# Optimization experiments

Measured on AMD Instinct MI355X. Metric: run time of the kernel, lower is better.

## Reference

```python
import jax, jax.numpy as jnp
import numpy as np

A_NUM = 9
C_NUM = 20

def setup_inputs() -> dict:
    key = jax.random.key(0)
    ks = jax.random.split(key, 12)
    B, Cin, H, W = 32, 256, 56, 56
    hidden = 256
    N, M = 64, 2048
    out_ch = 5 * A_NUM + C_NUM
    features = jax.random.normal(ks[0], (B, Cin, H, W), jnp.float32)
    w1 = jax.random.normal(ks[1], (hidden, Cin), jnp.float32) * (1.0 / np.sqrt(Cin))
    b1 = jax.random.normal(ks[2], (hidden,), jnp.float32) * 0.01
    w2 = jax.random.normal(ks[3], (out_ch, hidden), jnp.float32) * (1.0 / np.sqrt(hidden))
    b2 = jax.random.normal(ks[4], (out_ch,), jnp.float32) * 0.01
    # anchor shapes (w, h), positive sizes in grid units
    anc = 1.0 + 5.0 * jax.random.uniform(ks[5], (A_NUM, 2), jnp.float32)
    # grid of cell centers
    xs = jnp.arange(W, dtype=jnp.float32) + 0.5
    ys = jnp.arange(H, dtype=jnp.float32) + 0.5
    gx, gy = jnp.meshgrid(xs, ys, indexing='xy')  # (H, W)
    grid = jnp.broadcast_to(jnp.stack([gx, gy], axis=-1)[None], (B, H, W, 2))
    # GT boxes (x1, y1, x2, y2, cls) with x1<x2, y1<y2
    x1 = jax.random.uniform(ks[6], (B, N), jnp.float32) * (W - 9.0)
    y1 = jax.random.uniform(ks[7], (B, N), jnp.float32) * (H - 9.0)
    bw = 1.0 + 7.0 * jax.random.uniform(ks[8], (B, N), jnp.float32)
    bh = 1.0 + 7.0 * jax.random.uniform(ks[9], (B, N), jnp.float32)
    cls = jax.random.randint(ks[10], (B, N), 0, C_NUM).astype(jnp.float32)
    bboxes = jnp.stack([x1, y1, x1 + bw, y1 + bh, cls], axis=-1)
    total_anchors = B * A_NUM * H * W
    pos_anchor_idx = jax.random.randint(ks[11], (M,), 0, total_anchors, jnp.int64 if jax.config.jax_enable_x64 else jnp.int32)
    neg_anchor_idx = jax.random.randint(jax.random.fold_in(key, 99), (M,), 0, total_anchors, jnp.int64 if jax.config.jax_enable_x64 else jnp.int32)
    GT_offsets = jax.random.normal(jax.random.fold_in(key, 100), (M, 4), jnp.float32) * 0.1
    return {"features": features, "w1": w1, "b1": b1, "w2": w2, "b2": b2,
            "anc": anc, "grid": grid, "bboxes": bboxes, "GT_offsets": GT_offsets,
            "pos_anchor_idx": pos_anchor_idx, "neg_anchor_idx": neg_anchor_idx}

def _generate_anchor(anc, grid):
    # grid: (B,H,W,2), anc: (A,2) -> anchors (B,A,H,W,4) as (x1,y1,x2,y2)
    g = grid[:, None]                      # (B,1,H,W,2)
    a = anc[None, :, None, None]           # (1,A,1,1,2)
    return jnp.concatenate([g - a / 2, g + a / 2], axis=-1)

def _generate_proposal_yolo(anchors, offsets):
    ctr = (anchors[..., :2] + anchors[..., 2:]) / 2
    wh = anchors[..., 2:] - anchors[..., :2]
    new_wh = wh * jnp.exp(offsets[..., 2:])
    new_ctr = ctr + offsets[..., :2]
    return jnp.concatenate([new_ctr - new_wh / 2, new_ctr + new_wh / 2], axis=-1)

def _iou(proposals, bboxes):
    # proposals (B,A,H,W,4) -> (B,AHW,4); bboxes (B,N,5) -> iou (B,AHW,N)
    B = proposals.shape[0]
    p = proposals.reshape(B, -1, 4)[:, :, None, :]   # (B,AHW,1,4)
    g = bboxes[:, None, :, :]                        # (B,1,N,5)
    ix1 = jnp.maximum(p[..., 0], g[..., 0])
    iy1 = jnp.maximum(p[..., 1], g[..., 1])
    ix2 = jnp.minimum(p[..., 2], g[..., 2])
    iy2 = jnp.minimum(p[..., 3], g[..., 3])
    inter = jnp.clip(ix2 - ix1, 0) * jnp.clip(iy2 - iy1, 0)
    gt_area = (bboxes[:, :, 2] - bboxes[:, :, 0]) * (bboxes[:, :, 3] - bboxes[:, :, 1])
    p_area = (p[..., 2] - p[..., 0]) * (p[..., 3] - p[..., 1])
    return inter / (gt_area[:, None, :] + p_area - inter)

def reference(features, w1, b1, w2, b2, anc, grid, bboxes, GT_offsets,
              pos_anchor_idx, neg_anchor_idx):
    B, _, H, W = features.shape
    A = anc.shape[0]
    M = pos_anchor_idx.shape[0]
    # PredictionNetwork (dropout in eval = identity), 1x1 convs as einsum
    x = jnp.einsum('bchw,oc->bohw', features, w1) + b1[None, :, None, None]
    x = jax.nn.leaky_relu(x, 0.01)
    x = jnp.einsum('bchw,oc->bohw', x, w2) + b2[None, :, None, None]
    anc_data = x[:, :5 * A].reshape(B, A, 5, H, W)
    class_all = x[:, 5 * A:]                               # (B,C,H,W)
    conf_all = jax.nn.sigmoid(anc_data[:, :, 0])           # (B,A,H,W)
    offsets_all = jnp.transpose(anc_data[:, :, 1:5], (0, 1, 3, 4, 2))  # (B,A,H,W,4)
    # training extraction
    conf_flat = conf_all.reshape(-1)
    conf_scores = jnp.concatenate([conf_flat[pos_anchor_idx], conf_flat[neg_anchor_idx]])[:, None]  # (2M,1)
    offsets_pos = offsets_all.reshape(-1, 4)[pos_anchor_idx]            # (M,4)
    # class scores for positive anchors: index arithmetic over (B,A,H,W)
    bi = pos_anchor_idx // (A * H * W)
    hw = pos_anchor_idx % (H * W)
    hi, wi = hw // W, hw % W
    class_pos = class_all[bi, :, hi, wi]                                # (M,C)
    # anchors -> proposals -> IoU
    anchors = _generate_anchor(anc, grid)
    proposals = _generate_proposal_yolo(anchors, offsets_all)
    iou_mat = _iou(proposals, bboxes)                                   # (B,AHW,N)
    # YOLO SSE losses
    gt_conf = jnp.concatenate([jnp.ones((M, 1), conf_scores.dtype), jnp.zeros((M, 1), conf_scores.dtype)])
    conf_loss = jnp.sum((conf_scores - gt_conf) ** 2) / (2 * M)
    reg_loss = jnp.sum((offsets_pos - GT_offsets) ** 2) / M
    total_loss = conf_loss + reg_loss
    return total_loss, iou_mat, class_pos
```

## Files before the change

kernel.cpp:

```cpp
#include <hip/hip_runtime.h>
#include <math.h>

#define B_    32
#define CIN   256
#define HID   256
#define OC    65
#define A_    9
#define H_    56
#define W_    56
#define HW    3136
#define AHW   28224
#define NBOX  64
#define M_    2048
#define CNUM  20
#define NTILE 49
#define NTILES_TOT (B_ * NTILE)
#define NSLOT 25

#define IOU_N ((size_t)B_ * AHW * NBOX)

#define WS_W1S   0
#define WS_W2S   131072
#define WS_LOSS  172032
#define WS_PCNT  172288
#define WS_NCNT  178560
#define WS_PBUF  184832
#define WS_NBUF  586240

#define FOFF(frag) (((frag) << 3) + ((((frag) >> 3)) << 3))

typedef _Float16 half8 __attribute__((ext_vector_type(8)));
typedef float f32x16 __attribute__((ext_vector_type(16)));
typedef float f32x4  __attribute__((ext_vector_type(4)));

__device__ __forceinline__ unsigned int pkh(float a, float b) {
    _Float16 ha = (_Float16)a, hb = (_Float16)b;
    unsigned short ua = __builtin_bit_cast(unsigned short, ha);
    unsigned short ub = __builtin_bit_cast(unsigned short, hb);
    return (unsigned int)ua | ((unsigned int)ub << 16);
}

__device__ __forceinline__ void phase_barrier() {
    __builtin_amdgcn_sched_barrier(0);
    asm volatile("s_waitcnt lgkmcnt(0)" ::: "memory");
    __builtin_amdgcn_s_barrier();
    __builtin_amdgcn_sched_barrier(0);
}

__global__ __launch_bounds__(256) void zero_kernel(int* __restrict__ cnts,
                                                   float* __restrict__ loss_ws) {
    const int i = blockIdx.x * 256 + threadIdx.x;
    if (i < 2 * NTILES_TOT) cnts[i] = 0;
    if (i < 2) loss_ws[i] = 0.f;
}

__global__ __launch_bounds__(256) void prep_kernel(
    const float* __restrict__ w1, const float* __restrict__ w2,
    _Float16* __restrict__ w1s, _Float16* __restrict__ w2s,
    const int* __restrict__ pos_idx, const int* __restrict__ neg_idx,
    int* __restrict__ pcnt, int* __restrict__ ncnt,
    int* __restrict__ pbuf, int* __restrict__ nbuf)
{
    const int f = blockIdx.x * 256 + threadIdx.x;
    {
        const int e    = f & 7;
        const int lane = (f >> 3) & 63;
        const int kc   = (f >> 9) & 15;
        const int ob   = f >> 13;
        const int row  = ob * 32 + (lane & 31);
        const int k    = kc * 16 + (lane >> 5) * 8 + e;
        w1s[f] = (_Float16)w1[row * CIN + k];
    }
    if (f < 20480) {
        const int e    = f & 7;
        const int lane = (f >> 3) & 63;
        const int ks2  = (f >> 9) & 7;
        const int rt   = f >> 12;
        const int row  = rt * 16 + (lane & 15);
        const int k    = ks2 * 32 + (lane >> 4) * 8 + e;
        w2s[f] = (row < OC) ? (_Float16)w2[row * HID + k] : (_Float16)0.f;
    }
    if (f < 2 * M_) {
        const int m   = f & (M_ - 1);
        const int idx = (f < M_) ? pos_idx[m] : neg_idx[m];
        const int bi  = idx / AHW;
        const int rr  = idx - bi * AHW;
        const int a   = rr / HW;
        const int hw  = rr - a * HW;
        const int tile = bi * NTILE + (hw >> 6);
        const int enc  = m | (a << 11) | ((hw & 63) << 15);
        if (f < M_) {
            const int s = atomicAdd(&pcnt[tile], 1);
            if (s < 64) pbuf[tile * 64 + s] = enc;
        } else {
            const int s = atomicAdd(&ncnt[tile], 1);
            if (s < 64) nbuf[tile * 64 + s] = enc;
        }
    }
}

__device__ __forceinline__ void stage_issue(const float* __restrict__ fbase,
                                            int kk, int pstage,
                                            float4* __restrict__ s0,
                                            float4* __restrict__ s1)
{
#pragma unroll
    for (int c = 0; c < 8; ++c) {
        s0[c] = *(const float4*)(fbase + (size_t)(c * 32 + kk) * HW + pstage);
        s1[c] = *(const float4*)(fbase + (size_t)(c * 32 + kk + 1) * HW + pstage);
    }
}

__device__ __forceinline__ void stage_store(_Float16* __restrict__ featAll,
                                            int pstage, int ksS, int gS, int j0h,
                                            const float4* __restrict__ s0,
                                            const float4* __restrict__ s1)
{
#pragma unroll
    for (int c = 0; c < 8; ++c) {
        const float a0[4] = {s0[c].x, s0[c].y, s0[c].z, s0[c].w};
        const float a1[4] = {s1[c].x, s1[c].y, s1[c].z, s1[c].w};
#pragma unroll
        for (int e = 0; e < 4; ++e) {
            const int p     = pstage + e;
            const int lane2 = gS * 32 + (p & 31);
            const int pt    = p >> 5;
            const int frag  = c * 256 + (ksS * 2 + pt) * 64 + lane2;
            *(unsigned int*)&featAll[FOFF(frag) + j0h] = pkh(a0[e], a1[e]);
        }
    }
}

__global__ __launch_bounds__(256) void conv_iou_kernel(
    const float* __restrict__ features, const _Float16* __restrict__ w1s,
    const float* __restrict__ b1, const _Float16* __restrict__ w2s,
    const float* __restrict__ b2, const float* __restrict__ anc,
    const float* __restrict__ bboxes,
    const int* __restrict__ pcnt, const int* __restrict__ ncnt,
    const int* __restrict__ pbuf, const int* __restrict__ nbuf,
    const float* __restrict__ gt_off,
    float* __restrict__ iou_out, float* __restrict__ cls_out,
    float* __restrict__ loss_ws)
{
    __shared__ _Float16 lds_h[18432];
    __shared__ float bias_s[HID];
    __shared__ float boxs[5 * 64];
    __shared__ float red[8];

    _Float16* featAll = lds_h;
    _Float16* hidf    = lds_h;
    float*    L       = (float*)lds_h;
    float*    x2t     = L;

    const int t    = threadIdx.x;
    const int lane = t & 63;
    const int w    = t >> 6;
    const int bid  = blockIdx.x;
    const int b    = bid / NSLOT;
    const int slot = bid - b * NSLOT;
    const int j0t  = slot * 2;
    const int ntiles = (slot < NSLOT - 1) ? 2 : 1;
    const float* fb0 = features + (size_t)b * CIN * HW;

    float* WPw = L + 4416 + w * 720;

    bias_s[t] = b1[t];
    if (t < 64) {
        const float* gb = bboxes + ((size_t)b * NBOX + t) * 5;
        const float x1 = gb[0], y1 = gb[1], x2v = gb[2], y2v = gb[3];
        boxs[t] = x1; boxs[64 + t] = y1; boxs[128 + t] = x2v; boxs[192 + t] = y2v;
        boxs[256 + t] = (x2v - x1) * (y2v - y1);
    }

    const int pstage = (t & 15) * 4;
    const int kk     = (t >> 4) * 2;
    const int ksS    = kk >> 4;
    const int gS     = (kk >> 3) & 1;
    const int j0h    = kk & 7;
    const int ghalf  = lane >> 5;
    const int col    = lane & 31;
    const int m16    = lane & 15;
    const int kgr    = lane >> 4;
    const int pr     = lane >> 4;
    const int j0     = (lane & 15) * 4;

    float Bx1[4], By1[4], Bx2[4], By2[4], Ba[4];

    float4 s0[8], s1[8];
    stage_issue(fb0 + j0t * 64, kk, pstage, s0, s1);

    float csum = 0.f, rsum = 0.f;

    for (int it = 0; it < ntiles; ++it) {
        const int p0 = (j0t + it) * 64;

        stage_store(featAll, pstage, ksS, gS, j0h, s0, s1);
        phase_barrier();

        if (it == 0) {
#pragma unroll
            for (int e = 0; e < 4; ++e) {
                Bx1[e] = boxs[j0 + e];       By1[e] = boxs[64 + j0 + e];
                Bx2[e] = boxs[128 + j0 + e]; By2[e] = boxs[192 + j0 + e];
                Ba[e]  = boxs[256 + j0 + e];
            }
        }

        f32x16 facc[2][2];
#pragma unroll
        for (int ot = 0; ot < 2; ++ot)
#pragma unroll
            for (int pt = 0; pt < 2; ++pt)
#pragma unroll
                for (int e = 0; e < 16; ++e) facc[ot][pt][e] = 0.f;

        half8 afb[2][2][2];
#pragma unroll
        for (int ks = 0; ks < 2; ++ks)
#pragma unroll
            for (int ot = 0; ot < 2; ++ot)
                afb[0][ks][ot] = *(const half8*)(w1s + ((size_t)((w * 2 + ot) * 16 + ks) * 64 + lane) * 8);

#pragma unroll
        for (int c = 0; c < 8; ++c) {
            if (c < 7) {
#pragma unroll
                for (int ks = 0; ks < 2; ++ks)
#pragma unroll
                    for (int ot = 0; ot < 2; ++ot)
                        afb[(c + 1) & 1][ks][ot] =
                            *(const half8*)(w1s + ((size_t)((w * 2 + ot) * 16 + (c + 1) * 2 + ks) * 64 + lane) * 8);
            }
#pragma unroll
            for (int ks = 0; ks < 2; ++ks) {
#pragma unroll
                for (int pt = 0; pt < 2; ++pt) {
                    const half8 bf = *(const half8*)&featAll[FOFF(c * 256 + (ks * 2 + pt) * 64 + lane)];
                    facc[0][pt] = __builtin_amdgcn_mfma_f32_32x32x16_f16(afb[c & 1][ks][0], bf, facc[0][pt], 0, 0, 0);
                    facc[1][pt] = __builtin_amdgcn_mfma_f32_32x32x16_f16(afb[c & 1][ks][1], bf, facc[1][pt], 0, 0, 0);
                }
            }
        }
        phase_barrier();

#pragma unroll
        for (int ot = 0; ot < 2; ++ot) {
            const int ks2 = w * 2 + ot;
#pragma unroll
            for (int pt = 0; pt < 2; ++pt) {
                const int pt2 = pt * 2 + (col >> 4);
                const int n15 = col & 15;
#pragma unroll
                for (int q = 0; q < 4; ++q) {
                    float hv[4];
#pragma unroll
                    for (int i = 0; i < 4; ++i) {
                        const int row = i + 8 * q + 4 * ghalf;
                        float v = facc[ot][pt][q * 4 + i] + bias_s[w * 64 + ot * 32 + row];
                        hv[i] = v < 0.f ? 0.01f * v : v;
                    }
                    const int frag = (ks2 * 4 + pt2) * 64 + (q * 16 + n15);
                    *(unsigned int*)&hidf[FOFF(frag) + 4 * ghalf]     = pkh(hv[0], hv[1]);
                    *(unsigned int*)&hidf[FOFF(frag) + 4 * ghalf + 2] = pkh(hv[2], hv[3]);
                }
            }
        }
        phase_barrier();

        f32x4 c2[5];
#pragma unroll
        for (int rt = 0; rt < 5; ++rt)
#pragma unroll
            for (int e = 0; e < 4; ++e) c2[rt][e] = 0.f;

        half8 afc[2][5];
#pragma unroll
        for (int rt = 0; rt < 5; ++rt)
            afc[0][rt] = *(const half8*)(w2s + ((size_t)(rt * 8) * 64 + lane) * 8);

#pragma unroll
        for (int ks2 = 0; ks2 < 8; ++ks2) {
            if (ks2 < 7) {
#pragma unroll
                for (int rt = 0; rt < 5; ++rt)
                    afc[(ks2 + 1) & 1][rt] =
                        *(const half8*)(w2s + ((size_t)(rt * 8 + ks2 + 1) * 64 + lane) * 8);
            }
            const half8 bf = *(const half8*)&hidf[FOFF((ks2 * 4 + w) * 64 + lane)];
#pragma unroll
            for (int rt = 0; rt < 5; ++rt)
                c2[rt] = __builtin_amdgcn_mfma_f32_16x16x32_f16(afc[ks2 & 1][rt], bf, c2[rt], 0, 0, 0);
        }

        if (it + 1 < ntiles)
            stage_issue(fb0 + (p0 + 64), kk, pstage, s0, s1);

        phase_barrier();

        const int pxl = w * 16 + m16;
#pragma unroll
        for (int rt = 0; rt < 5; ++rt) {
#pragma unroll
            for (int r = 0; r < 4; ++r) {
                const int o2 = rt * 16 + kgr * 4 + r;
                if (o2 < OC) x2t[pxl * 69 + o2] = c2[rt][r] + b2[o2];
            }
        }
        asm volatile("" ::: "memory");

        for (int i = lane; i < A_ * 16; i += 64) {
            const int a  = i >> 4;
            const int pw = i & 15;
            const float* xr = x2t + (w * 16 + pw) * 69 + 5 * a;
            const float tx = xr[1], ty = xr[2], tw = xr[3], th = xr[4];
            const int hwg = p0 + w * 16 + pw;
            const int h   = hwg / W_;
            const int wv  = hwg - h * W_;
            const float gx = (float)wv + 0.5f;
            const float gy = (float)h + 0.5f;
            const float nw = anc[2 * a]     * __expf(tw);
            const float nh = anc[2 * a + 1] * __expf(th);
            const float cx = gx + tx, cy = gy + ty;
            WPw[i]       = cx - 0.5f * nw;
            WPw[144 + i] = cy - 0.5f * nh;
            WPw[288 + i] = cx + 0.5f * nw;
            WPw[432 + i] = cy + 0.5f * nh;
            WPw[576 + i] = nw * nh;
        }
        asm volatile("" ::: "memory");

        float* ibase = iou_out + ((size_t)b * AHW + p0) * 64;
#pragma unroll 1
        for (int a = 0; a < A_; ++a) {
            float Px1[4], Py1[4], Px2[4], Py2[4], Pa[4];
#pragma unroll
            for (int q = 0; q < 4; ++q) {
                const int idx = a * 16 + q * 4 + pr;
                Px1[q] = WPw[idx];       Py1[q] = WPw[144 + idx];
                Px2[q] = WPw[288 + idx]; Py2[q] = WPw[432 + idx];
                Pa[q]  = WPw[576 + idx];
            }
#pragma unroll
            for (int q = 0; q < 4; ++q) {
                f32x4 o4;
#pragma unroll
                for (int e = 0; e < 4; ++e) {
                    const float iw = fminf(Px2[q], Bx2[e]) - fmaxf(Px1[q], Bx1[e]);
                    const float ih = fminf(Py2[q], By2[e]) - fmaxf(Py1[q], By1[e]);
                    const float inter = fmaxf(iw, 0.f) * fmaxf(ih, 0.f);
                    o4[e] = inter * __builtin_amdgcn_rcpf(Ba[e] + Pa[q] - inter);
                }
                *(f32x4*)(ibase + ((size_t)(a * HW) + w * 16 + q * 4 + pr) * 64 + j0) = o4;
            }
        }

        phase_barrier();

        {
            const int bidt = b * NTILE + j0t + it;
            int np = pcnt[bidt]; np = np > 64 ? 64 : np;
            for (int i = t; i < np; i += 256) {
                const int e  = pbuf[bidt * 64 + i];
                const int m  = e & 2047;
                const int a  = (e >> 11) & 15;
                const int px = (e >> 15) & 63;
                const float* xr = x2t + px * 69;
                const float s = 1.f / (1.f + __expf(-xr[5 * a]));
                csum += (s - 1.f) * (s - 1.f);
#pragma unroll
                for (int k = 0; k < 4; ++k) {
                    const float d = xr[5 * a + 1 + k] - gt_off[m * 4 + k];
                    rsum += d * d;
                }
                float* co = cls_out + (size_t)m * CNUM;
#pragma unroll
                for (int c = 0; c < CNUM; ++c) co[c] = xr[45 + c];
            }
            int nn = ncnt[bidt]; nn = nn > 64 ? 64 : nn;
            for (int i = t; i < nn; i += 256) {
                const int e  = nbuf[bidt * 64 + i];
                const int a  = (e >> 11) & 15;
                const int px = (e >> 15) & 63;
                const float s = 1.f / (1.f + __expf(-x2t[px * 69 + 5 * a]));
                csum += s * s;
            }
        }
        phase_barrier();
    }

#pragma unroll
    for (int off = 32; off > 0; off >>= 1) {
        csum += __shfl_down(csum, off, 64);
        rsum += __shfl_down(rsum, off, 64);
    }
    if (lane == 0) { red[w] = csum; red[4 + w] = rsum; }
    __syncthreads();
    if (t == 0) {
        const float c  = red[0] + red[1] + red[2] + red[3];
        const float rg = red[4] + red[5] + red[6] + red[7];
        if (c != 0.f || rg != 0.f) {
            atomicAdd(&loss_ws[0], c);
            atomicAdd(&loss_ws[1], rg);
        }
    }
}

__global__ void finalize_kernel(const float* __restrict__ loss_ws, float* __restrict__ out0)
{
    out0[0] = loss_ws[0] / (2.f * (float)M_) + loss_ws[1] / (float)M_;
}

extern "C" void kernel_launch(void* const* d_in, const int* in_sizes, int n_in,
                              void* d_out, int out_size, void* d_ws, size_t ws_size,
                              hipStream_t stream) {
    (void)in_sizes; (void)n_in; (void)out_size; (void)ws_size;
    const float* features = (const float*)d_in[0];
    const float* w1       = (const float*)d_in[1];
    const float* b1       = (const float*)d_in[2];
    const float* w2       = (const float*)d_in[3];
    const float* b2       = (const float*)d_in[4];
    const float* anc      = (const float*)d_in[5];
    const float* bboxes   = (const float*)d_in[7];
    const float* gt_off   = (const float*)d_in[8];
    const int*   pos_idx  = (const int*)d_in[9];
    const int*   neg_idx  = (const int*)d_in[10];
    float* out = (float*)d_out;

    char* wsb = (char*)d_ws;
    _Float16* w1s  = (_Float16*)(wsb + WS_W1S);
    _Float16* w2s  = (_Float16*)(wsb + WS_W2S);
    float* loss_ws = (float*)(wsb + WS_LOSS);
    int*   pcnt    = (int*)(wsb + WS_PCNT);
    int*   ncnt    = (int*)(wsb + WS_NCNT);
    int*   pbuf    = (int*)(wsb + WS_PBUF);
    int*   nbuf    = (int*)(wsb + WS_NBUF);

    zero_kernel<<<13, 256, 0, stream>>>(pcnt, loss_ws);
    prep_kernel<<<256, 256, 0, stream>>>(w1, w2, w1s, w2s, pos_idx, neg_idx,
                                         pcnt, ncnt, pbuf, nbuf);
    conv_iou_kernel<<<B_ * NSLOT, 256, 0, stream>>>(features, w1s, b1, w2s, b2,
                                                    anc, bboxes, pcnt, ncnt, pbuf, nbuf,
                                                    gt_off, out + 1,
                                                    out + 1 + IOU_N, loss_ws);
    finalize_kernel<<<1, 1, 0, stream>>>(loss_ws, out);
}
```

Before: 432.3 us.

## Restructure fused conv kernel to one tile per block with per-wave pixel split

Each block now handles a single 64-pixel tile (1568 blocks) rather than two tiles with software prefetch of the next tile's features. Layer 1 switches from 32x32 MFMAs split over output channels to 16x16x32 MFMAs where each wave owns 16 pixels and all 256 hidden channels. The hidden activations are passed to layer 2 through cross-lane shuffles in registers, which removes the LDS round trip and several block barriers. The feature staging layout gains an XOR swizzle to cut LDS bank conflicts. In exchange, each wave now reads all of W1 from global/L2 with no double buffering, and per-thread register pressure rises from 64 accumulators.

```diff
diff --git a/kernel.cpp b/kernel.cpp
--- a/kernel.cpp
+++ b/kernel.cpp
@@ -15,7 +15,6 @@
 #define CNUM  20
 #define NTILE 49
 #define NTILES_TOT (B_ * NTILE)
-#define NSLOT 25
 
 #define IOU_N ((size_t)B_ * AHW * NBOX)
 
@@ -27,10 +26,7 @@
 #define WS_PBUF  184832
 #define WS_NBUF  586240
 
-#define FOFF(frag) (((frag) << 3) + ((((frag) >> 3)) << 3))
-
 typedef _Float16 half8 __attribute__((ext_vector_type(8)));
-typedef float f32x16 __attribute__((ext_vector_type(16)));
 typedef float f32x4  __attribute__((ext_vector_type(4)));
 
 __device__ __forceinline__ unsigned int pkh(float a, float b) {
@@ -40,12 +36,7 @@
     return (unsigned int)ua | ((unsigned int)ub << 16);
 }
 
-__device__ __forceinline__ void phase_barrier() {
-    __builtin_amdgcn_sched_barrier(0);
-    asm volatile("s_waitcnt lgkmcnt(0)" ::: "memory");
-    __builtin_amdgcn_s_barrier();
-    __builtin_amdgcn_sched_barrier(0);
-}
+__device__ __forceinline__ int swz(int h) { return h ^ (((h >> 12) & 3) << 4); }
 
 __global__ __launch_bounds__(256) void zero_kernel(int* __restrict__ cnts,
                                                    float* __restrict__ loss_ws) {
@@ -65,10 +56,10 @@
     {
         const int e    = f & 7;
         const int lane = (f >> 3) & 63;
-        const int kc   = (f >> 9) & 15;
-        const int ob   = f >> 13;
-        const int row  = ob * 32 + (lane & 31);
-        const int k    = kc * 16 + (lane >> 5) * 8 + e;
+        const int ks   = (f >> 9) & 7;
+        const int rt   = (f >> 12) & 15;
+        const int row  = rt * 16 + (lane & 15);
+        const int k    = ks * 32 + (lane >> 4) * 8 + e;
         w1s[f] = (_Float16)w1[row * CIN + k];
     }
     if (f < 20480) {
@@ -99,38 +90,6 @@
     }
 }
 
-__device__ __forceinline__ void stage_issue(const float* __restrict__ fbase,
-                                            int kk, int pstage,
-                                            float4* __restrict__ s0,
-                                            float4* __restrict__ s1)
-{
-#pragma unroll
-    for (int c = 0; c < 8; ++c) {
-        s0[c] = *(const float4*)(fbase + (size_t)(c * 32 + kk) * HW + pstage);
-        s1[c] = *(const float4*)(fbase + (size_t)(c * 32 + kk + 1) * HW + pstage);
-    }
-}
-
-__device__ __forceinline__ void stage_store(_Float16* __restrict__ featAll,
-                                            int pstage, int ksS, int gS, int j0h,
-                                            const float4* __restrict__ s0,
-                                            const float4* __restrict__ s1)
-{
-#pragma unroll
-    for (int c = 0; c < 8; ++c) {
-        const float a0[4] = {s0[c].x, s0[c].y, s0[c].z, s0[c].w};
-        const float a1[4] = {s1[c].x, s1[c].y, s1[c].z, s1[c].w};
-#pragma unroll
-        for (int e = 0; e < 4; ++e) {
-            const int p     = pstage + e;
-            const int lane2 = gS * 32 + (p & 31);
-            const int pt    = p >> 5;
-            const int frag  = c * 256 + (ksS * 2 + pt) * 64 + lane2;
-            *(unsigned int*)&featAll[FOFF(frag) + j0h] = pkh(a0[e], a1[e]);
-        }
-    }
-}
-
 __global__ __launch_bounds__(256) void conv_iou_kernel(
     const float* __restrict__ features, const _Float16* __restrict__ w1s,
     const float* __restrict__ b1, const _Float16* __restrict__ w2s,
@@ -142,29 +101,22 @@
     float* __restrict__ iou_out, float* __restrict__ cls_out,
     float* __restrict__ loss_ws)
 {
-    __shared__ _Float16 lds_h[18432];
-    __shared__ float bias_s[HID];
+    __shared__ _Float16 lds_h[16384];
     __shared__ float boxs[5 * 64];
     __shared__ float red[8];
 
-    _Float16* featAll = lds_h;
-    _Float16* hidf    = lds_h;
-    float*    L       = (float*)lds_h;
-    float*    x2t     = L;
+    float* LF = (float*)lds_h;
 
     const int t    = threadIdx.x;
     const int lane = t & 63;
     const int w    = t >> 6;
+    const int g    = lane >> 4;
+    const int m16  = lane & 15;
     const int bid  = blockIdx.x;
-    const int b    = bid / NSLOT;
-    const int slot = bid - b * NSLOT;
-    const int j0t  = slot * 2;
-    const int ntiles = (slot < NSLOT - 1) ? 2 : 1;
-    const float* fb0 = features + (size_t)b * CIN * HW;
-
-    float* WPw = L + 4416 + w * 720;
-
-    bias_s[t] = b1[t];
+    const int b    = bid / NTILE;
+    const int p0   = (bid - b * NTILE) * 64;
+    const float* fbase = features + (size_t)b * CIN * HW + p0;
+
     if (t < 64) {
         const float* gb = bboxes + ((size_t)b * NBOX + t) * 5;
         const float x1 = gb[0], y1 = gb[1], x2v = gb[2], y2v = gb[3];
@@ -174,220 +126,192 @@
 
     const int pstage = (t & 15) * 4;
     const int kk     = (t >> 4) * 2;
-    const int ksS    = kk >> 4;
-    const int gS     = (kk >> 3) & 1;
-    const int j0h    = kk & 7;
-    const int ghalf  = lane >> 5;
-    const int col    = lane & 31;
-    const int m16    = lane & 15;
-    const int kgr    = lane >> 4;
-    const int pr     = lane >> 4;
-    const int j0     = (lane & 15) * 4;
-
+#pragma unroll
+    for (int hf = 0; hf < 2; ++hf) {
+        float4 r0[4], r1[4];
+#pragma unroll
+        for (int c4 = 0; c4 < 4; ++c4) {
+            const int c = hf * 4 + c4;
+            r0[c4] = *(const float4*)(fbase + (size_t)(c * 32 + kk) * HW + pstage);
+            r1[c4] = *(const float4*)(fbase + (size_t)(c * 32 + kk + 1) * HW + pstage);
+        }
+#pragma unroll
+        for (int c4 = 0; c4 < 4; ++c4) {
+            const int c = hf * 4 + c4;
+            const float a0[4] = {r0[c4].x, r0[c4].y, r0[c4].z, r0[c4].w};
+            const float a1[4] = {r1[c4].x, r1[c4].y, r1[c4].z, r1[c4].w};
+#pragma unroll
+            for (int e = 0; e < 4; ++e) {
+                const int p = pstage + e;
+                const int W = ((p >> 4) * 8 + c) * 512
+                            + (((kk >> 3) & 3) * 16 + (p & 15)) * 8 + (kk & 7);
+                *(unsigned int*)&lds_h[swz(W)] = pkh(a0[e], a1[e]);
+            }
+        }
+    }
+    __syncthreads();
+
+    f32x4 facc[16];
+#pragma unroll
+    for (int rt = 0; rt < 16; ++rt)
+#pragma unroll
+        for (int e = 0; e < 4; ++e) facc[rt][e] = 0.f;
+
+#pragma unroll
+    for (int ks = 0; ks < 8; ++ks) {
+        const half8 bf = *(const half8*)&lds_h[swz(((w * 8 + ks) * 64 + lane) * 8)];
+#pragma unroll
+        for (int rt = 0; rt < 16; ++rt) {
+            const half8 af = *(const half8*)(w1s + ((size_t)(rt * 8 + ks) * 64 + lane) * 8);
+            facc[rt] = __builtin_amdgcn_mfma_f32_16x16x32_f16(af, bf, facc[rt], 0, 0, 0);
+        }
+    }
+
+    unsigned hvpk[8][4];
+#pragma unroll
+    for (int rt2 = 0; rt2 < 8; ++rt2) {
+        const float4 bA = *(const float4*)(b1 + (2 * rt2) * 16 + g * 4);
+        const float4 bB = *(const float4*)(b1 + (2 * rt2 + 1) * 16 + g * 4);
+        const float bav[4] = {bA.x, bA.y, bA.z, bA.w};
+        const float bbv[4] = {bB.x, bB.y, bB.z, bB.w};
+#pragma unroll
+        for (int r = 0; r < 4; ++r) {
+            float va = facc[2 * rt2][r] + bav[r];
+            float vb = facc[2 * rt2 + 1][r] + bbv[r];
+            va = va < 0.f ? 0.01f * va : va;
+            vb = vb < 0.f ? 0.01f * vb : vb;
+            hvpk[rt2][r] = pkh(va, vb);
+        }
+    }
+
+    f32x4 c2[5];
+#pragma unroll
+    for (int rt = 0; rt < 5; ++rt)
+#pragma unroll
+        for (int e = 0; e < 4; ++e) c2[rt][e] = 0.f;
+
+    const int src0 = (g & 1) * 32 + m16;
+    const int sh   = (g >> 1) * 16;
+#pragma unroll
+    for (int ks2 = 0; ks2 < 8; ++ks2) {
+        unsigned u[8];
+#pragma unroll
+        for (int j = 0; j < 8; ++j)
+            u[j] = (unsigned)__shfl((int)hvpk[ks2][j & 3], (j < 4) ? src0 : src0 + 16);
+        union { unsigned q[4]; half8 h; } bu;
+#pragma unroll
+        for (int wd = 0; wd < 4; ++wd)
+            bu.q[wd] = ((u[2 * wd] >> sh) & 0xffffu) | (((u[2 * wd + 1] >> sh) & 0xffffu) << 16);
+#pragma unroll
+        for (int rt = 0; rt < 5; ++rt) {
+            const half8 af = *(const half8*)(w2s + ((size_t)(rt * 8 + ks2) * 64 + lane) * 8);
+            c2[rt] = __builtin_amdgcn_mfma_f32_16x16x32_f16(af, bu.h, c2[rt], 0, 0, 0);
+        }
+    }
+    asm volatile("" ::: "memory");
+
+    float* xw = LF + w * 2048;
+#pragma unroll
+    for (int rt = 0; rt < 5; ++rt) {
+#pragma unroll
+        for (int r = 0; r < 4; ++r) {
+            const int o2 = rt * 16 + g * 4 + r;
+            if (o2 < OC) xw[m16 * 69 + o2] = c2[rt][r] + b2[o2];
+        }
+    }
+    asm volatile("" ::: "memory");
+
+    float* WPw = LF + w * 2048 + 1104;
+    for (int i = lane; i < A_ * 16; i += 64) {
+        const int a  = i >> 4;
+        const int pw = i & 15;
+        const float* xr = xw + pw * 69 + 5 * a;
+        const float tx = xr[1], ty = xr[2], tw = xr[3], th = xr[4];
+        const int hwg = p0 + w * 16 + pw;
+        const int h   = hwg / W_;
+        const int wv  = hwg - h * W_;
+        const float gx = (float)wv + 0.5f;
+        const float gy = (float)h + 0.5f;
+        const float nw = anc[2 * a]     * __expf(tw);
+        const float nh = anc[2 * a + 1] * __expf(th);
+        const float cx = gx + tx, cy = gy + ty;
+        WPw[i]       = cx - 0.5f * nw;
+        WPw[144 + i] = cy - 0.5f * nh;
+        WPw[288 + i] = cx + 0.5f * nw;
+        WPw[432 + i] = cy + 0.5f * nh;
+        WPw[576 + i] = nw * nh;
+    }
+    asm volatile("" ::: "memory");
+
+    const int pr = g;
+    const int j0 = m16 * 4;
     float Bx1[4], By1[4], Bx2[4], By2[4], Ba[4];
-
-    float4 s0[8], s1[8];
-    stage_issue(fb0 + j0t * 64, kk, pstage, s0, s1);
+#pragma unroll
+    for (int e = 0; e < 4; ++e) {
+        Bx1[e] = boxs[j0 + e];       By1[e] = boxs[64 + j0 + e];
+        Bx2[e] = boxs[128 + j0 + e]; By2[e] = boxs[192 + j0 + e];
+        Ba[e]  = boxs[256 + j0 + e];
+    }
+    float* ibase = iou_out + ((size_t)b * AHW + p0) * 64;
+#pragma unroll 1
+    for (int a = 0; a < A_; ++a) {
+        float Px1[4], Py1[4], Px2[4], Py2[4], Pa[4];
+#pragma unroll
+        for (int q = 0; q < 4; ++q) {
+            const int idx = a * 16 + q * 4 + pr;
+            Px1[q] = WPw[idx];       Py1[q] = WPw[144 + idx];
+            Px2[q] = WPw[288 + idx]; Py2[q] = WPw[432 + idx];
+            Pa[q]  = WPw[576 + idx];
+        }
+#pragma unroll
+        for (int q = 0; q < 4; ++q) {
+            f32x4 o4;
+#pragma unroll
+            for (int e = 0; e < 4; ++e) {
+                const float iw = fminf(Px2[q], Bx2[e]) - fmaxf(Px1[q], Bx1[e]);
+                const float ih = fminf(Py2[q], By2[e]) - fmaxf(Py1[q], By1[e]);
+                const float inter = fmaxf(iw, 0.f) * fmaxf(ih, 0.f);
+                o4[e] = inter * __builtin_amdgcn_rcpf(Ba[e] + Pa[q] - inter);
+            }
+            *(f32x4*)(ibase + ((size_t)(a * HW) + w * 16 + q * 4 + pr) * 64 + j0) = o4;
+        }
+    }
+
+    __builtin_amdgcn_sched_barrier(0);
+    asm volatile("s_waitcnt lgkmcnt(0)" ::: "memory");
+    __builtin_amdgcn_s_barrier();
+    __builtin_amdgcn_sched_barrier(0);
 
     float csum = 0.f, rsum = 0.f;
-
-    for (int it = 0; it < ntiles; ++it) {
-        const int p0 = (j0t + it) * 64;
-
-        stage_store(featAll, pstage, ksS, gS, j0h, s0, s1);
-        phase_barrier();
-
-        if (it == 0) {
-#pragma unroll
-            for (int e = 0; e < 4; ++e) {
-                Bx1[e] = boxs[j0 + e];       By1[e] = boxs[64 + j0 + e];
-                Bx2[e] = boxs[128 + j0 + e]; By2[e] = boxs[192 + j0 + e];
-                Ba[e]  = boxs[256 + j0 + e];
+    {
+        int np = pcnt[bid]; np = np > 64 ? 64 : np;
+        for (int i = t; i < np; i += 256) {
+            const int e  = pbuf[bid * 64 + i];
+            const int m  = e & 2047;
+            const int a  = (e >> 11) & 15;
+            const int px = (e >> 15) & 63;
+            const float* xr = LF + (px >> 4) * 2048 + (px & 15) * 69;
+            const float s = 1.f / (1.f + __expf(-xr[5 * a]));
+            csum += (s - 1.f) * (s - 1.f);
+#pragma unroll
+            for (int k = 0; k < 4; ++k) {
+                const float d = xr[5 * a + 1 + k] - gt_off[m * 4 + k];
+                rsum += d * d;
             }
-        }
-
-        f32x16 facc[2][2];
-#pragma unroll
-        for (int ot = 0; ot < 2; ++ot)
-#pragma unroll
-            for (int pt = 0; pt < 2; ++pt)
-#pragma unroll
-                for (int e = 0; e < 16; ++e) facc[ot][pt][e] = 0.f;
-
-        half8 afb[2][2][2];
-#pragma unroll
-        for (int ks = 0; ks < 2; ++ks)
-#pragma unroll
-            for (int ot = 0; ot < 2; ++ot)
-                afb[0][ks][ot] = *(const half8*)(w1s + ((size_t)((w * 2 + ot) * 16 + ks) * 64 + lane) * 8);
-
-#pragma unroll
-        for (int c = 0; c < 8; ++c) {
-            if (c < 7) {
-#pragma unroll
-                for (int ks = 0; ks < 2; ++ks)
-#pragma unroll
-                    for (int ot = 0; ot < 2; ++ot)
-                        afb[(c + 1) & 1][ks][ot] =
-                            *(const half8*)(w1s + ((size_t)((w * 2 + ot) * 16 + (c + 1) * 2 + ks) * 64 + lane) * 8);
-            }
-#pragma unroll
-            for (int ks = 0; ks < 2; ++ks) {
-#pragma unroll
-                for (int pt = 0; pt < 2; ++pt) {
-                    const half8 bf = *(const half8*)&featAll[FOFF(c * 256 + (ks * 2 + pt) * 64 + lane)];
-                    facc[0][pt] = __builtin_amdgcn_mfma_f32_32x32x16_f16(afb[c & 1][ks][0], bf, facc[0][pt], 0, 0, 0);
-                    facc[1][pt] = __builtin_amdgcn_mfma_f32_32x32x16_f16(afb[c & 1][ks][1], bf, facc[1][pt], 0, 0, 0);
-                }
-            }
-        }
-        phase_barrier();
-
-#pragma unroll
-        for (int ot = 0; ot < 2; ++ot) {
-            const int ks2 = w * 2 + ot;
-#pragma unroll
-            for (int pt = 0; pt < 2; ++pt) {
-                const int pt2 = pt * 2 + (col >> 4);
-                const int n15 = col & 15;
-#pragma unroll
-                for (int q = 0; q < 4; ++q) {
-                    float hv[4];
-#pragma unroll
-                    for (int i = 0; i < 4; ++i) {
-                        const int row = i + 8 * q + 4 * ghalf;
-                        float v = facc[ot][pt][q * 4 + i] + bias_s[w * 64 + ot * 32 + row];
-                        hv[i] = v < 0.f ? 0.01f * v : v;
-                    }
-                    const int frag = (ks2 * 4 + pt2) * 64 + (q * 16 + n15);
-                    *(unsigned int*)&hidf[FOFF(frag) + 4 * ghalf]     = pkh(hv[0], hv[1]);
-                    *(unsigned int*)&hidf[FOFF(frag) + 4 * ghalf + 2] = pkh(hv[2], hv[3]);
-                }
-            }
-        }
-        phase_barrier();
-
-        f32x4 c2[5];
-#pragma unroll
-        for (int rt = 0; rt < 5; ++rt)
-#pragma unroll
-            for (int e = 0; e < 4; ++e) c2[rt][e] = 0.f;
-
-        half8 afc[2][5];
-#pragma unroll
-        for (int rt = 0; rt < 5; ++rt)
-            afc[0][rt] = *(const half8*)(w2s + ((size_t)(rt * 8) * 64 + lane) * 8);
-
-#pragma unroll
-        for (int ks2 = 0; ks2 < 8; ++ks2) {
-            if (ks2 < 7) {
-#pragma unroll
-                for (int rt = 0; rt < 5; ++rt)
-                    afc[(ks2 + 1) & 1][rt] =
-                        *(const half8*)(w2s + ((size_t)(rt * 8 + ks2 + 1) * 64 + lane) * 8);
-            }
-            const half8 bf = *(const half8*)&hidf[FOFF((ks2 * 4 + w) * 64 + lane)];
-#pragma unroll
-            for (int rt = 0; rt < 5; ++rt)
-                c2[rt] = __builtin_amdgcn_mfma_f32_16x16x32_f16(afc[ks2 & 1][rt], bf, c2[rt], 0, 0, 0);
-        }
-
-        if (it + 1 < ntiles)
-            stage_issue(fb0 + (p0 + 64), kk, pstage, s0, s1);
-
-        phase_barrier();
-
-        const int pxl = w * 16 + m16;
-#pragma unroll
-        for (int rt = 0; rt < 5; ++rt) {
-#pragma unroll
-            for (int r = 0; r < 4; ++r) {
-                const int o2 = rt * 16 + kgr * 4 + r;
-                if (o2 < OC) x2t[pxl * 69 + o2] = c2[rt][r] + b2[o2];
-            }
-        }
-        asm volatile("" ::: "memory");
-
-        for (int i = lane; i < A_ * 16; i += 64) {
-            const int a  = i >> 4;
-            const int pw = i & 15;
-            const float* xr = x2t + (w * 16 + pw) * 69 + 5 * a;
-            const float tx = xr[1], ty = xr[2], tw = xr[3], th = xr[4];
-            const int hwg = p0 + w * 16 + pw;
-            const int h   = hwg / W_;
-            const int wv  = hwg - h * W_;
-            const float gx = (float)wv + 0.5f;
-            const float gy = (float)h + 0.5f;
-            const float nw = anc[2 * a]     * __expf(tw);
-            const float nh = anc[2 * a + 1] * __expf(th);
-            const float cx = gx + tx, cy = gy + ty;
-            WPw[i]       = cx - 0.5f * nw;
-            WPw[144 + i] = cy - 0.5f * nh;
-            WPw[288 + i] = cx + 0.5f * nw;
-            WPw[432 + i] = cy + 0.5f * nh;
-            WPw[576 + i] = nw * nh;
-        }
-        asm volatile("" ::: "memory");
-
-        float* ibase = iou_out + ((size_t)b * AHW + p0) * 64;
-#pragma unroll 1
-        for (int a = 0; a < A_; ++a) {
-            float Px1[4], Py1[4], Px2[4], Py2[4], Pa[4];
-#pragma unroll
-            for (int q = 0; q < 4; ++q) {
-                const int idx = a * 16 + q * 4 + pr;
-                Px1[q] = WPw[idx];       Py1[q] = WPw[144 + idx];
-                Px2[q] = WPw[288 + idx]; Py2[q] = WPw[432 + idx];
-                Pa[q]  = WPw[576 + idx];
-            }
-#pragma unroll
-            for (int q = 0; q < 4; ++q) {
-                f32x4 o4;
-#pragma unroll
-                for (int e = 0; e < 4; ++e) {
-                    const float iw = fminf(Px2[q], Bx2[e]) - fmaxf(Px1[q], Bx1[e]);
-                    const float ih = fminf(Py2[q], By2[e]) - fmaxf(Py1[q], By1[e]);
-                    const float inter = fmaxf(iw, 0.f) * fmaxf(ih, 0.f);
-                    o4[e] = inter * __builtin_amdgcn_rcpf(Ba[e] + Pa[q] - inter);
-                }
-                *(f32x4*)(ibase + ((size_t)(a * HW) + w * 16 + q * 4 + pr) * 64 + j0) = o4;
-            }
-        }
-
-        phase_barrier();
-
-        {
-            const int bidt = b * NTILE + j0t + it;
-            int np = pcnt[bidt]; np = np > 64 ? 64 : np;
-            for (int i = t; i < np; i += 256) {
-                const int e  = pbuf[bidt * 64 + i];
-                const int m  = e & 2047;
-                const int a  = (e >> 11) & 15;
-                const int px = (e >> 15) & 63;
-                const float* xr = x2t + px * 69;
-                const float s = 1.f / (1.f + __expf(-xr[5 * a]));
-                csum += (s - 1.f) * (s - 1.f);
-#pragma unroll
-                for (int k = 0; k < 4; ++k) {
-                    const float d = xr[5 * a + 1 + k] - gt_off[m * 4 + k];
-                    rsum += d * d;
-                }
-                float* co = cls_out + (size_t)m * CNUM;
-#pragma unroll
-                for (int c = 0; c < CNUM; ++c) co[c] = xr[45 + c];
-            }
-            int nn = ncnt[bidt]; nn = nn > 64 ? 64 : nn;
-            for (int i = t; i < nn; i += 256) {
-                const int e  = nbuf[bidt * 64 + i];
-                const int a  = (e >> 11) & 15;
-                const int px = (e >> 15) & 63;
-                const float s = 1.f / (1.f + __expf(-x2t[px * 69 + 5 * a]));
-                csum += s * s;
-            }
-        }
-        phase_barrier();
-    }
-
+            float* co = cls_out + (size_t)m * CNUM;
+#pragma unroll
+            for (int c = 0; c < CNUM; ++c) co[c] = xr[45 + c];
+        }
+        int nn = ncnt[bid]; nn = nn > 64 ? 64 : nn;
+        for (int i = t; i < nn; i += 256) {
+            const int e  = nbuf[bid * 64 + i];
+            const int a  = (e >> 11) & 15;
+            const int px = (e >> 15) & 63;
+            const float* xr = LF + (px >> 4) * 2048 + (px & 15) * 69;
+            const float s = 1.f / (1.f + __expf(-xr[5 * a]));
+            csum += s * s;
+        }
+    }
 #pragma unroll
     for (int off = 32; off > 0; off >>= 1) {
         csum += __shfl_down(csum, off, 64);
@@ -438,7 +362,7 @@
     zero_kernel<<<13, 256, 0, stream>>>(pcnt, loss_ws);
     prep_kernel<<<256, 256, 0, stream>>>(w1, w2, w1s, w2s, pos_idx, neg_idx,
                                          pcnt, ncnt, pbuf, nbuf);
-    conv_iou_kernel<<<B_ * NSLOT, 256, 0, stream>>>(features, w1s, b1, w2s, b2,
+    conv_iou_kernel<<<NTILES_TOT, 256, 0, stream>>>(features, w1s, b1, w2s, b2,
                                                     anc, bboxes, pcnt, ncnt, pbuf, nbuf,
                                                     gt_off, out + 1,
                                                     out + 1 + IOU_N, loss_ws);
```

New measurement: 506.0 us. +17.0%, slower.
